# Performance work log

Hardware: AMD Instinct MI355X
Metric: run time of the kernel (lower is better)

## Reference

```python
import jax, jax.numpy as jnp
import numpy as np

HEADS = 8
DIM_HEAD = 64
CHUNK = 128
EPS = 1e-6
KERNEL_EPS = 1e-4


def softmax_kernel(x, proj, is_query):
    # x: [b,h,n,d], proj: [f,d]  (FAVOR+ positive softmax features)
    d = x.shape[-1]
    data_normalizer = d ** -0.25
    ratio = proj.shape[0] ** -0.5
    data_dash = jnp.einsum('bhnd,fd->bhnf', x * data_normalizer, proj)
    diag = 0.5 * (data_normalizer ** 2) * jnp.sum(x * x, axis=-1, keepdims=True)  # [b,h,n,1]
    if is_query:
        m = jnp.max(data_dash, axis=-1, keepdims=True)
    else:
        m = jnp.max(data_dash, axis=(-1, -2), keepdims=True)
    return ratio * (jnp.exp(data_dash - diag - jax.lax.stop_gradient(m)) + KERNEL_EPS)


def infer_hidden_states(q, k, v, chunk_size=CHUNK):
    # q,k: [b,h,n,f], v: [b,h,n,e]; chunked causal linear attention with carried cumsums
    b, h, n, f = q.shape
    e = v.shape[-1]
    nc = n // chunk_size

    def to_chunks(t):
        return jnp.moveaxis(t.reshape(b, h, nc, chunk_size, t.shape[-1]), 2, 0)

    qs, ks, vs = to_chunks(q), to_chunks(k), to_chunks(v)

    def step(carry, inp):
        Z, S = carry  # [b,h,1,f], [b,h,1,f,e]
        qc, kc, vc = inp
        k_cum = Z + jnp.cumsum(kc, axis=2)                       # [b,h,c,f]
        D_inv = 1.0 / jnp.einsum('bhnf,bhnf->bhn', qc, k_cum + EPS)
        ctx = jnp.einsum('bhnf,bhne->bhnfe', kc, vc)             # [b,h,c,f,e]
        ctx_cum = S + jnp.cumsum(ctx, axis=2)
        out = jnp.einsum('bhnfe,bhnf,bhn->bhne', ctx_cum, qc, D_inv)
        return (k_cum[:, :, -1:], ctx_cum[:, :, -1:]), out

    init = (jnp.zeros((b, h, 1, f), q.dtype), jnp.zeros((b, h, 1, f, e), q.dtype))
    (Z, S), outs = jax.lax.scan(step, init, (qs, ks, vs))
    out = jnp.moveaxis(outs, 0, 2).reshape(b, h, n, e)
    return out, Z[:, :, 0], S[:, :, 0]


def reference(x, proj, Wq, Wk, Wv, Wo, bo):
    b, n, dim = x.shape
    h, dh = HEADS, DIM_HEAD

    def split_heads(t):
        return jnp.transpose(t.reshape(b, n, h, dh), (0, 2, 1, 3))

    q = split_heads(x @ Wq)
    k = split_heads(x @ Wk)
    v = split_heads(x @ Wv)

    qf = softmax_kernel(q, proj, is_query=True)
    kf = softmax_kernel(k, proj, is_query=False)

    out, Z, S = infer_hidden_states(qf, kf, v)
    out = jnp.transpose(out, (0, 2, 1, 3)).reshape(b, n, h * dh)
    out = out @ Wo + bo
    return out, Z, S


def setup_inputs() -> dict:
    key = jax.random.key(0)
    ks = jax.random.split(key, 6)
    b, n, dim = 2, 2048, 512
    f = 256
    return {
        'x': jax.random.normal(ks[0], (b, n, dim), jnp.float32),
        'proj': jax.random.normal(ks[1], (f, DIM_HEAD), jnp.float32),
        'Wq': jax.random.normal(ks[2], (dim, dim), jnp.float32) * (dim ** -0.5),
        'Wk': jax.random.normal(ks[3], (dim, dim), jnp.float32) * (dim ** -0.5),
        'Wv': jax.random.normal(ks[4], (dim, dim), jnp.float32) * (dim ** -0.5),
        'Wo': jax.random.normal(ks[5], (dim, dim), jnp.float32) * (dim ** -0.5),
        'bo': jnp.zeros((dim,), jnp.float32),
    }
```

## Files before the change

kernel.cpp:

```cpp
#include <hip/hip_runtime.h>
#include <hip/hip_bf16.h>
#include <math.h>

#define NB    2
#define NSEQ  2048
#define DIMM  512
#define NH    8
#define DHd   64
#define FF    256
#define CHK   128
#define NCHK  16
#define NBH   16

typedef unsigned short ushort_t;
typedef __attribute__((ext_vector_type(8))) __bf16 bf16x8;
typedef __attribute__((ext_vector_type(4))) float floatx4;

__device__ __forceinline__ unsigned short f2bf(float x) {
    union { __hip_bfloat16 h; unsigned short u; } v;
    v.h = __float2bfloat16(x);
    return v.u;
}
__device__ __forceinline__ float bf2f(unsigned short u) {
    union { unsigned short u2[2]; float f; } v;
    v.u2[0] = 0; v.u2[1] = u;
    return v.f;
}
__device__ __forceinline__ unsigned enc_f(float x) {
    unsigned u = __float_as_uint(x);
    return (u & 0x80000000u) ? ~u : (u | 0x80000000u);
}
__device__ __forceinline__ float dec_f(unsigned e) {
    unsigned u = (e & 0x80000000u) ? (e & 0x7fffffffu) : ~e;
    return __uint_as_float(u);
}

__device__ __forceinline__ void gload16(const void* g, void* l) {
    __builtin_amdgcn_global_load_lds(
        (const __attribute__((address_space(1))) void*)g,
        (__attribute__((address_space(3))) void*)l, 16, 0, 0);
}

__device__ __forceinline__ bf16x8 frag8(const ushort_t* lds, int row, int kb) {
    return *((const bf16x8*)lds + row * 8 + (kb ^ (row & 7)));
}
__device__ __forceinline__ bf16x8 fragS(const ushort_t* lds, int row, int kb) {
    return *((const bf16x8*)lds + row * 16 + (kb ^ (row & 15)));
}

__global__ __launch_bounds__(256)
void prep(const float* __restrict__ x, const float* __restrict__ proj,
          const float* __restrict__ W0, const float* __restrict__ W1,
          const float* __restrict__ W2, const float* __restrict__ W3,
          ushort_t* __restrict__ xb, ushort_t* __restrict__ projb,
          ushort_t* __restrict__ T0, ushort_t* __restrict__ T1,
          ushort_t* __restrict__ T2, ushort_t* __restrict__ T3,
          unsigned* __restrict__ mk_u)
{
    __shared__ float t[32][33];
    const int b = blockIdx.x, tid = threadIdx.x;
    if (b < 2048) {
        const int gid = b * 256 + tid;
        const float4 v = *(const float4*)(x + (size_t)gid * 4);
        union { ushort4 v4; unsigned short s[4]; } pk;
        pk.s[0] = f2bf(v.x); pk.s[1] = f2bf(v.y); pk.s[2] = f2bf(v.z); pk.s[3] = f2bf(v.w);
        ((ushort4*)xb)[gid] = pk.v4;
    } else if (b < 2064) {
        const int gid = (b - 2048) * 256 + tid;
        const float dn = 0.35355339059327379f;
        const float4 v = *(const float4*)(proj + (size_t)gid * 4);
        union { ushort4 v4; unsigned short s[4]; } pk;
        pk.s[0] = f2bf(v.x * dn); pk.s[1] = f2bf(v.y * dn);
        pk.s[2] = f2bf(v.z * dn); pk.s[3] = f2bf(v.w * dn);
        ((ushort4*)projb)[gid] = pk.v4;
    } else if (b < 3088) {
        const int idx = b - 2064;
        const int z = idx >> 8, rem = idx & 255;
        const int bx = rem & 15, by = rem >> 4;
        const float* W = (z == 0) ? W0 : (z == 1) ? W1 : (z == 2) ? W2 : W3;
        ushort_t* T = (z == 0) ? T0 : (z == 1) ? T1 : (z == 2) ? T2 : T3;
        const int x0 = bx * 32, y0 = by * 32;
        const int tx = tid & 31, ty = tid >> 5;
#pragma unroll
        for (int i = 0; i < 4; i++)
            t[ty + i * 8][tx] = W[(size_t)(y0 + ty + i * 8) * DIMM + x0 + tx];
        __syncthreads();
#pragma unroll
        for (int i = 0; i < 4; i++)
            T[(size_t)(x0 + ty + i * 8) * DIMM + y0 + tx] = f2bf(t[tx][ty + i * 8]);
    } else {
        if (tid < NBH) mk_u[tid] = 0u;
    }
}

__device__ __forceinline__ void mfma_mainloop(
    const ushort_t* __restrict__ AG, const ushort_t* __restrict__ BG,
    ushort_t* As, ushort_t* Bs, int ldA, int ldB, int K,
    floatx4 acc[4][4], int tid)
{
    const int lane = tid & 63, wid = tid >> 6;
    const int q = lane >> 4, c = lane & 15;
    const int wm = (wid >> 1) * 64, wn = (wid & 1) * 64;

    for (int k0 = 0; k0 < K; k0 += 64) {
#pragma unroll
        for (int t = 0; t < 4; t++) {
            const int g = t * 256 + tid, r = g >> 3, kb = (g & 7) ^ (r & 7);
            gload16(AG + (size_t)r * ldA + k0 + kb * 8, As + (size_t)g * 8);
        }
#pragma unroll
        for (int t = 0; t < 4; t++) {
            const int g = t * 256 + tid, r = g >> 3, kb = (g & 7) ^ (r & 7);
            gload16(BG + (size_t)r * ldB + k0 + kb * 8, Bs + (size_t)g * 8);
        }
        __syncthreads();
#pragma unroll
        for (int ks = 0; ks < 2; ks++) {
            bf16x8 af[4], bfr[4];
#pragma unroll
            for (int i = 0; i < 4; i++) {
                af[i]  = frag8(As, wm + i * 16 + c, ks * 4 + q);
                bfr[i] = frag8(Bs, wn + i * 16 + c, ks * 4 + q);
            }
#pragma unroll
            for (int i = 0; i < 4; i++)
#pragma unroll
                for (int j = 0; j < 4; j++)
                    acc[i][j] = __builtin_amdgcn_mfma_f32_16x16x32_bf16(
                        af[i], bfr[j], acc[i][j], 0, 0, 0);
        }
        __syncthreads();
    }
}

__global__ __launch_bounds__(256)
void gemm_qkv(const ushort_t* __restrict__ xb,
              const ushort_t* __restrict__ Wtq, const ushort_t* __restrict__ Wtk,
              const ushort_t* __restrict__ Wtv,
              ushort_t* __restrict__ qb, ushort_t* __restrict__ kb,
              ushort_t* __restrict__ vTb)
{
    __shared__ alignas(16) ushort_t SM[16896];
    ushort_t* As = SM;
    ushort_t* Bs = SM + 8192;
    const int tid = threadIdx.x;
    const int n0 = blockIdx.x * 128, m0 = blockIdx.y * 128, z = blockIdx.z;
    const ushort_t* Bt = (z == 0) ? Wtq : ((z == 1) ? Wtk : Wtv);

    floatx4 zero = {0.f, 0.f, 0.f, 0.f};
    floatx4 acc[4][4];
#pragma unroll
    for (int i = 0; i < 4; i++)
#pragma unroll
        for (int j = 0; j < 4; j++) acc[i][j] = zero;

    mfma_mainloop(xb + (size_t)m0 * DIMM, Bt + (size_t)n0 * DIMM, As, Bs,
                  DIMM, DIMM, DIMM, acc, tid);

    const int lane = tid & 63, wid = tid >> 6;
    const int q = lane >> 4, c = lane & 15;
    const int wm = (wid >> 1) * 64, wn = (wid & 1) * 64;

#pragma unroll
    for (int i = 0; i < 4; i++)
#pragma unroll
        for (int j = 0; j < 4; j++) {
            const int col = wn + j * 16 + c;
#pragma unroll
            for (int r = 0; r < 4; r++) {
                const int row = wm + i * 16 + q * 4 + r;
                SM[row * 132 + col] = f2bf(acc[i][j][r]);
            }
        }
    __syncthreads();

    if (z < 2) {
        ushort_t* ob = (z == 0) ? qb : kb;
#pragma unroll
        for (int p = 0; p < 16; p++) {
            const int idx = p * 256 + tid;
            const int row = idx >> 5, c4 = idx & 31;
            ushort4 o = *(const ushort4*)&SM[row * 132 + c4 * 4];
            *(ushort4*)(ob + (size_t)(m0 + row) * DIMM + n0 + c4 * 4) = o;
        }
    } else {
        const int bb = m0 >> 11, nbase = m0 & 2047;
#pragma unroll
        for (int p = 0; p < 16; p++) {
            const int idx = p * 256 + tid;
            const int cl2 = idx >> 5, n4 = idx & 31;
            const int C = n0 + cl2;
            const int h = C >> 6, e = C & 63;
            union { ushort4 v4; unsigned short s[4]; } pk;
#pragma unroll
            for (int k = 0; k < 4; k++) pk.s[k] = SM[(n4 * 4 + k) * 132 + cl2];
            *(ushort4*)(vTb + (((size_t)(bb * NH + h) * 64 + e)) * NSEQ + nbase + n4 * 4) = pk.v4;
        }
    }
}

__global__ __launch_bounds__(256)
void gemm_out(const ushort_t* __restrict__ attnb, const ushort_t* __restrict__ Wto,
              float* __restrict__ out, const float* __restrict__ bias)
{
    __shared__ alignas(16) ushort_t As[8192];
    __shared__ alignas(16) ushort_t Bs[8192];
    const int tid = threadIdx.x;
    const int n0 = blockIdx.x * 128, m0 = blockIdx.y * 128;

    floatx4 zero = {0.f, 0.f, 0.f, 0.f};
    floatx4 acc[4][4];
#pragma unroll
    for (int i = 0; i < 4; i++)
#pragma unroll
        for (int j = 0; j < 4; j++) acc[i][j] = zero;

    mfma_mainloop(attnb + (size_t)m0 * DIMM, Wto + (size_t)n0 * DIMM, As, Bs,
                  DIMM, DIMM, DIMM, acc, tid);

    const int lane = tid & 63, wid = tid >> 6;
    const int q = lane >> 4, c = lane & 15;
    const int wm = (wid >> 1) * 64, wn = (wid & 1) * 64;
#pragma unroll
    for (int i = 0; i < 4; i++)
#pragma unroll
        for (int j = 0; j < 4; j++) {
            const int col = n0 + wn + j * 16 + c;
            const float bv = bias[col];
#pragma unroll
            for (int r = 0; r < 4; r++) {
                const int row = m0 + wm + i * 16 + q * 4 + r;
                out[(size_t)row * DIMM + col] = acc[i][j][r] + bv;
            }
        }
}

__global__ __launch_bounds__(256)
void kmax(const ushort_t* __restrict__ kb_, const ushort_t* __restrict__ projb,
          unsigned* __restrict__ mk_u)
{
    __shared__ alignas(16) ushort_t As[8192];
    __shared__ alignas(16) ushort_t Bs[16384];
    __shared__ float red[256];
    const int tid = threadIdx.x, lane = tid & 63, wid = tid >> 6;
    const int q = lane >> 4, cl = lane & 15;
    const int m0 = blockIdx.x * 128, h = blockIdx.y;
    const int bb = m0 >> 11;
    const ushort_t* Aq = kb_ + (size_t)m0 * DIMM + h * 64;

#pragma unroll
    for (int t = 0; t < 4; t++) {
        const int g = t * 256 + tid, r = g >> 3, kb = (g & 7) ^ (r & 7);
        gload16(Aq + (size_t)r * DIMM + kb * 8, As + (size_t)g * 8);
    }
#pragma unroll
    for (int t = 0; t < 8; t++) {
        const int g = t * 256 + tid, r = g >> 3, kb = (g & 7) ^ (r & 7);
        gload16(projb + (size_t)r * 64 + kb * 8, Bs + (size_t)g * 8);
    }
    __syncthreads();

    floatx4 zero = {0.f, 0.f, 0.f, 0.f};
    floatx4 acc[4][8];
#pragma unroll
    for (int i = 0; i < 4; i++)
#pragma unroll
        for (int j = 0; j < 8; j++) acc[i][j] = zero;
    const int wm = (wid >> 1) * 64, wn = (wid & 1) * 128;
#pragma unroll
    for (int ks = 0; ks < 2; ks++) {
        bf16x8 af[4], bfr[8];
#pragma unroll
        for (int i = 0; i < 4; i++) af[i] = frag8(As, wm + i * 16 + cl, ks * 4 + q);
#pragma unroll
        for (int j = 0; j < 8; j++) bfr[j] = frag8(Bs, wn + j * 16 + cl, ks * 4 + q);
#pragma unroll
        for (int i = 0; i < 4; i++)
#pragma unroll
            for (int j = 0; j < 8; j++)
                acc[i][j] = __builtin_amdgcn_mfma_f32_16x16x32_bf16(
                    af[i], bfr[j], acc[i][j], 0, 0, 0);
    }
    float mloc = -3.0e38f;
#pragma unroll
    for (int i = 0; i < 4; i++)
#pragma unroll
        for (int j = 0; j < 8; j++)
#pragma unroll
            for (int r = 0; r < 4; r++) mloc = fmaxf(mloc, acc[i][j][r]);
    red[tid] = mloc;
    __syncthreads();
    for (int s = 128; s > 0; s >>= 1) {
        if (tid < s) red[tid] = fmaxf(red[tid], red[tid + s]);
        __syncthreads();
    }
    if (tid == 0) atomicMax(&mk_u[bb * NH + h], enc_f(red[0]));
}

__global__ __launch_bounds__(256)
void featx(const ushort_t* __restrict__ qb_, const ushort_t* __restrict__ kb_,
           const ushort_t* __restrict__ projb, const unsigned* __restrict__ mk_u,
           const ushort_t* __restrict__ vTb,
           ushort_t* __restrict__ qfb, ushort_t* __restrict__ kfb,
           float* __restrict__ CTXT, float* __restrict__ Ksum)
{
    __shared__ alignas(16) ushort_t SM[24576];
    __shared__ float dtmp[256];
    __shared__ float diag_l[128];
    __shared__ float mx2[2][128];
    __shared__ float colp[2][256];
    ushort_t* As = SM;
    ushort_t* Bs = SM + 8192;
    const int tid = threadIdx.x, lane = tid & 63, wid = tid >> 6;
    const int q = lane >> 4, cl = lane & 15;
    const int m0 = blockIdx.x * 128, h = blockIdx.y, src = blockIdx.z;
    const int bb = m0 >> 11, nloc = m0 & 2047;
    const int bh = bb * NH + h;
    const int cidx = nloc >> 7;
    const ushort_t* Aq = (src ? kb_ : qb_) + (size_t)m0 * DIMM + h * 64;

    {
        const int row = tid >> 1, half = tid & 1;
        float s = 0.f;
        const ushort_t* p = Aq + (size_t)row * DIMM + half * 32;
#pragma unroll
        for (int d = 0; d < 32; d += 4) {
            ushort4 w = *(const ushort4*)(p + d);
            float a = bf2f(w.x), b2 = bf2f(w.y), c2 = bf2f(w.z), d2 = bf2f(w.w);
            s += a * a + b2 * b2 + c2 * c2 + d2 * d2;
        }
        dtmp[tid] = s;
    }
    __syncthreads();
    if (tid < 128) diag_l[tid] = (dtmp[2 * tid] + dtmp[2 * tid + 1]) * 0.0625f;

#pragma unroll
    for (int t = 0; t < 4; t++) {
        const int g = t * 256 + tid, r = g >> 3, kb = (g & 7) ^ (r & 7);
        gload16(Aq + (size_t)r * DIMM + kb * 8, As + (size_t)g * 8);
    }
#pragma unroll
    for (int t = 0; t < 8; t++) {
        const int g = t * 256 + tid, r = g >> 3, kb = (g & 7) ^ (r & 7);
        gload16(projb + (size_t)r * 64 + kb * 8, Bs + (size_t)g * 8);
    }
    __syncthreads();

    floatx4 zero = {0.f, 0.f, 0.f, 0.f};
    floatx4 acc[4][8];
#pragma unroll
    for (int i = 0; i < 4; i++)
#pragma unroll
        for (int j = 0; j < 8; j++) acc[i][j] = zero;
    const int wm = (wid >> 1) * 64, wn = (wid & 1) * 128;
#pragma unroll
    for (int ks = 0; ks < 2; ks++) {
        bf16x8 af[4], bfr[8];
#pragma unroll
        for (int i = 0; i < 4; i++) af[i] = frag8(As, wm + i * 16 + cl, ks * 4 + q);
#pragma unroll
        for (int j = 0; j < 8; j++) bfr[j] = frag8(Bs, wn + j * 16 + cl, ks * 4 + q);
#pragma unroll
        for (int i = 0; i < 4; i++)
#pragma unroll
            for (int j = 0; j < 8; j++)
                acc[i][j] = __builtin_amdgcn_mfma_f32_16x16x32_bf16(
                    af[i], bfr[j], acc[i][j], 0, 0, 0);
    }

    const float mk = src ? dec_f(mk_u[bh]) : 0.f;
    if (src == 0) {
#pragma unroll
        for (int i = 0; i < 4; i++)
#pragma unroll
            for (int r = 0; r < 4; r++) {
                const int row = wm + i * 16 + q * 4 + r;
                float mx = -3.0e38f;
#pragma unroll
                for (int j = 0; j < 8; j++) mx = fmaxf(mx, acc[i][j][r]);
                mx = fmaxf(mx, __shfl_xor(mx, 1)); mx = fmaxf(mx, __shfl_xor(mx, 2));
                mx = fmaxf(mx, __shfl_xor(mx, 4)); mx = fmaxf(mx, __shfl_xor(mx, 8));
                if (cl == 0) mx2[wid & 1][row] = mx;
            }
    }
    __syncthreads();

#pragma unroll
    for (int i = 0; i < 4; i++)
#pragma unroll
        for (int r = 0; r < 4; r++) {
            const int row = wm + i * 16 + q * 4 + r;
            const float cc = diag_l[row] + (src ? mk : fmaxf(mx2[0][row], mx2[1][row]));
#pragma unroll
            for (int j = 0; j < 8; j++)
                acc[i][j][r] = 0.0625f * (__expf(acc[i][j][r] - cc) + 1.0e-4f);
        }

    if (src) {
#pragma unroll
        for (int j = 0; j < 8; j++) {
            float s = 0.f;
#pragma unroll
            for (int i = 0; i < 4; i++)
                s += acc[i][j][0] + acc[i][j][1] + acc[i][j][2] + acc[i][j][3];
            s += __shfl_xor(s, 16);
            s += __shfl_xor(s, 32);
            if (q == 0) colp[wid >> 1][wn + j * 16 + cl] = s;
        }
    }

    ushort_t* ff = src ? kfb : qfb;
    const size_t frow = (size_t)bh * NSEQ + nloc;

#pragma unroll
    for (int hf = 0; hf < 2; hf++) {
        __syncthreads();
        if ((wid & 1) == hf) {
#pragma unroll
            for (int i = 0; i < 4; i++)
#pragma unroll
                for (int j = 0; j < 8; j++) {
                    const int col = j * 16 + cl;
#pragma unroll
                    for (int r = 0; r < 4; r++) {
                        const int row = wm + i * 16 + q * 4 + r;
                        SM[row * 132 + col] = f2bf(acc[i][j][r]);
                    }
                }
        }
        if (hf == 0 && src) {
            Ksum[((size_t)bh * NCHK + cidx) * FF + tid] = colp[0][tid] + colp[1][tid];
        }
        __syncthreads();
#pragma unroll
        for (int p = 0; p < 16; p++) {
            const int idx = p * 256 + tid;
            const int row = idx >> 5, c4 = idx & 31;
            ushort4 o = *(const ushort4*)&SM[row * 132 + c4 * 4];
            *(ushort4*)(ff + (frow + row) * FF + hf * 128 + c4 * 4) = o;
        }
    }

    if (src == 0) return;

    __syncthreads();
    ushort_t* Vs = SM;
    ushort_t* T  = SM + 8192;
    const ushort_t* Vg = vTb + ((size_t)bh * 64) * NSEQ + nloc;
#pragma unroll
    for (int t = 0; t < 4; t++) {
        const int g = t * 256 + tid, r = g >> 4, kb = (g & 15) ^ (r & 15);
        gload16(Vg + (size_t)r * NSEQ + kb * 8, Vs + (size_t)g * 8);
    }

    const size_t cbase = ((size_t)bh * NCHK + cidx) * 64;
#pragma unroll
    for (int fq = 0; fq < 4; fq++) {
        if ((wid & 1) == (fq >> 1)) {
#pragma unroll
            for (int jj = 0; jj < 4; jj++) {
                const int j = (fq & 1) * 4 + jj;
#pragma unroll
                for (int i = 0; i < 4; i++)
#pragma unroll
                    for (int r = 0; r < 4; r++) {
                        const int n = wm + i * 16 + q * 4 + r;
                        T[(jj * 16 + cl) * 136 + n] = f2bf(acc[i][j][r]);
                    }
            }
        }
        __syncthreads();
        floatx4 accc[4];
#pragma unroll
        for (int jj = 0; jj < 4; jj++) accc[jj] = zero;
#pragma unroll
        for (int kt = 0; kt < 4; kt++) {
            const bf16x8 av = fragS(Vs, wid * 16 + cl, kt * 4 + q);
#pragma unroll
            for (int jj = 0; jj < 4; jj++) {
                const bf16x8 bv = *(const bf16x8*)(T + (jj * 16 + cl) * 136 + (kt * 4 + q) * 8);
                accc[jj] = __builtin_amdgcn_mfma_f32_16x16x32_bf16(av, bv, accc[jj], 0, 0, 0);
            }
        }
#pragma unroll
        for (int jj = 0; jj < 4; jj++) {
            const int f = fq * 64 + jj * 16 + cl;
#pragma unroll
            for (int r = 0; r < 4; r++) {
                const int e = wid * 16 + q * 4 + r;
                CTXT[(cbase + e) * FF + f] = accc[jj][r];
            }
        }
        __syncthreads();
    }
}

__global__ void prefix_zs(float* __restrict__ Ksum, float* __restrict__ Zout,
                          const float* __restrict__ CTXT, ushort_t* __restrict__ ctxp,
                          float* __restrict__ Sout)
{
    const int b = blockIdx.x;
    if (b < 1024) {
        const int idx = b * 256 + threadIdx.x;
        const int bh = idx >> 14, ef = idx & 16383;
        const int e = ef >> 8, f = ef & 255;
        float run = 0.f;
#pragma unroll
        for (int c = 0; c < NCHK; c++) {
            const size_t o = (((size_t)bh * NCHK + c) * 64 + e) * FF + f;
            const float t = CTXT[o];
            ctxp[o] = f2bf(run);
            run += t;
        }
        Sout[((size_t)bh * FF + f) * 64 + e] = run;
    } else {
        const int idx = (b - 1024) * 256 + threadIdx.x;
        const int bh = idx >> 8, f = idx & 255;
        float run = 0.f;
#pragma unroll
        for (int c = 0; c < NCHK; c++) {
            const size_t o = ((size_t)(bh * NCHK + c)) * FF + f;
            const float t = Ksum[o];
            Ksum[o] = run;
            run += t;
        }
        Zout[(size_t)bh * FF + f] = run;
    }
}

__global__ __launch_bounds__(256)
void chunk_out_mfma(const ushort_t* __restrict__ qfb, const ushort_t* __restrict__ kfb,
                    const ushort_t* __restrict__ vTb, const float* __restrict__ Zex,
                    const ushort_t* __restrict__ ctxp, ushort_t* __restrict__ attnb)
{
    __shared__ alignas(16) ushort_t Sld[16384];
    __shared__ alignas(16) ushort_t As[8192];
    __shared__ alignas(16) ushort_t Bs[8192];
    __shared__ float zeps[256];
    __shared__ float rows_part[2][128];
    __shared__ float denp[256];
    __shared__ float den_l[128];

    const int tid = threadIdx.x, lane = tid & 63, wid = tid >> 6;
    const int q = lane >> 4, cl = lane & 15;
    const int bh = blockIdx.x >> 4, c = blockIdx.x & 15;
    const int bb = bh >> 3, h = bh & 7;
    const int n0 = c * CHK;
    const ushort_t* Q  = qfb + ((size_t)bh * NSEQ + n0) * FF;
    const ushort_t* Kf = kfb + ((size_t)bh * NSEQ + n0) * FF;

    zeps[tid] = Zex[((size_t)bh * NCHK + c) * FF + tid] + 1.0e-6f;

    floatx4 zero = {0.f, 0.f, 0.f, 0.f};
    floatx4 acc1[4][4];
#pragma unroll
    for (int i = 0; i < 4; i++)
#pragma unroll
        for (int j = 0; j < 4; j++) acc1[i][j] = zero;
    const int wm = (wid >> 1) * 64, wn = (wid & 1) * 64;
    for (int k0 = 0; k0 < FF; k0 += 64) {
#pragma unroll
        for (int t = 0; t < 4; t++) {
            const int g = t * 256 + tid, r = g >> 3, kb = (g & 7) ^ (r & 7);
            gload16(Q + (size_t)r * FF + k0 + kb * 8, As + (size_t)g * 8);
        }
#pragma unroll
        for (int t = 0; t < 4; t++) {
            const int g = t * 256 + tid, r = g >> 3, kb = (g & 7) ^ (r & 7);
            gload16(Kf + (size_t)r * FF + k0 + kb * 8, Bs + (size_t)g * 8);
        }
        __syncthreads();
#pragma unroll
        for (int ks = 0; ks < 2; ks++) {
            bf16x8 af[4], bfr[4];
#pragma unroll
            for (int i = 0; i < 4; i++) {
                af[i]  = frag8(As, wm + i * 16 + cl, ks * 4 + q);
                bfr[i] = frag8(Bs, wn + i * 16 + cl, ks * 4 + q);
            }
#pragma unroll
            for (int i = 0; i < 4; i++)
#pragma unroll
                for (int j = 0; j < 4; j++)
                    acc1[i][j] = __builtin_amdgcn_mfma_f32_16x16x32_bf16(
                        af[i], bfr[j], acc1[i][j], 0, 0, 0);
        }
        __syncthreads();
    }
#pragma unroll
    for (int i = 0; i < 4; i++)
#pragma unroll
        for (int r = 0; r < 4; r++) {
            const int row = wm + i * 16 + q * 4 + r;
            float part = 0.f;
#pragma unroll
            for (int j = 0; j < 4; j++) {
                const int col = wn + j * 16 + cl;
                const float v = (col <= row) ? acc1[i][j][r] : 0.f;
                part += v;
                Sld[(row * 16 + ((col >> 3) ^ (row & 15))) * 8 + (col & 7)] = f2bf(v);
            }
            part += __shfl_xor(part, 1); part += __shfl_xor(part, 2);
            part += __shfl_xor(part, 4); part += __shfl_xor(part, 8);
            if (cl == 0) rows_part[wid & 1][row] = part;
        }
    __syncthreads();

    floatx4 acc2[4][2];
#pragma unroll
    for (int i = 0; i < 4; i++)
#pragma unroll
        for (int j = 0; j < 2; j++) acc2[i][j] = zero;
    const ushort_t* Vt = vTb + ((size_t)bh * 64) * NSEQ + n0;
    for (int k0 = 0; k0 < CHK; k0 += 64) {
#pragma unroll
        for (int t = 0; t < 2; t++) {
            const int g = t * 256 + tid, r = g >> 3, kb = (g & 7) ^ (r & 7);
            gload16(Vt + (size_t)r * NSEQ + k0 + kb * 8, As + (size_t)g * 8);
        }
        __syncthreads();
#pragma unroll
        for (int ks = 0; ks < 2; ks++) {
            bf16x8 af[4], bfr[2];
            const int kbS = (k0 >> 3) + ks * 4 + q;
#pragma unroll
            for (int i = 0; i < 4; i++) af[i] = frag8(As, i * 16 + cl, ks * 4 + q);
#pragma unroll
            for (int j = 0; j < 2; j++) bfr[j] = fragS(Sld, wid * 32 + j * 16 + cl, kbS);
#pragma unroll
            for (int i = 0; i < 4; i++)
#pragma unroll
                for (int j = 0; j < 2; j++)
                    acc2[i][j] = __builtin_amdgcn_mfma_f32_16x16x32_bf16(
                        af[i], bfr[j], acc2[i][j], 0, 0, 0);
        }
        __syncthreads();
    }

    const ushort_t* Cp = ctxp + ((size_t)bh * NCHK + c) * 64 * FF;
    float dacc = 0.f;
    const int drow = tid & 127, dhalf = tid >> 7;
    for (int k0 = 0; k0 < FF; k0 += 64) {
#pragma unroll
        for (int t = 0; t < 2; t++) {
            const int g = t * 256 + tid, r = g >> 3, kb = (g & 7) ^ (r & 7);
            gload16(Cp + (size_t)r * FF + k0 + kb * 8, As + (size_t)g * 8);
        }
#pragma unroll
        for (int t = 0; t < 4; t++) {
            const int g = t * 256 + tid, r = g >> 3, kb = (g & 7) ^ (r & 7);
            gload16(Q + (size_t)r * FF + k0 + kb * 8, Bs + (size_t)g * 8);
        }
        __syncthreads();
#pragma unroll
        for (int ks = 0; ks < 2; ks++) {
            bf16x8 af[4], bfr[2];
#pragma unroll
            for (int i = 0; i < 4; i++) af[i] = frag8(As, i * 16 + cl, ks * 4 + q);
#pragma unroll
            for (int j = 0; j < 2; j++) bfr[j] = frag8(Bs, wid * 32 + j * 16 + cl, ks * 4 + q);
#pragma unroll
            for (int i = 0; i < 4; i++)
#pragma unroll
                for (int j = 0; j < 2; j++)
                    acc2[i][j] = __builtin_amdgcn_mfma_f32_16x16x32_bf16(
                        af[i], bfr[j], acc2[i][j], 0, 0, 0);
        }
#pragma unroll
        for (int gi = 0; gi < 4; gi++) {
            const int kb = dhalf * 4 + gi;
            const ushort_t* gp = Bs + ((size_t)drow * 8 + (kb ^ (drow & 7))) * 8;
            const int kbase = k0 + kb * 8;
#pragma unroll
            for (int e2 = 0; e2 < 8; e2++)
                dacc = fmaf(bf2f(gp[e2]), zeps[kbase + e2], dacc);
        }
        __syncthreads();
    }
    denp[tid] = dacc;
    __syncthreads();
    if (tid < 128)
        den_l[tid] = rows_part[0][tid] + rows_part[1][tid] + denp[tid] + denp[tid + 128];
    __syncthreads();

#pragma unroll
    for (int j = 0; j < 2; j++) {
        const int row = wid * 32 + j * 16 + cl;
        const float dinv = 1.0f / den_l[row];
#pragma unroll
        for (int i = 0; i < 4; i++)
#pragma unroll
            for (int r = 0; r < 4; r++) {
                const int e = i * 16 + q * 4 + r;
                Sld[row * 68 + e] = f2bf(acc2[i][j][r] * dinv);
            }
    }
    __syncthreads();
#pragma unroll
    for (int p = 0; p < 8; p++) {
        const int idx = p * 256 + tid;
        const int row = idx >> 4, e4 = idx & 15;
        ushort4 o = *(const ushort4*)&Sld[row * 68 + e4 * 4];
        *(ushort4*)(attnb + ((size_t)(bb * NSEQ + n0 + row)) * DIMM + h * 64 + e4 * 4) = o;
    }
}

extern "C" void kernel_launch(void* const* d_in, const int* in_sizes, int n_in,
                              void* d_out, int out_size, void* d_ws, size_t ws_size,
                              hipStream_t stream)
{
    (void)in_sizes; (void)n_in; (void)out_size; (void)ws_size;
    const float* x    = (const float*)d_in[0];
    const float* proj = (const float*)d_in[1];
    const float* Wq   = (const float*)d_in[2];
    const float* Wk   = (const float*)d_in[3];
    const float* Wv   = (const float*)d_in[4];
    const float* Wo   = (const float*)d_in[5];
    const float* bo   = (const float*)d_in[6];
    float* out = (float*)d_out;

    char* W = (char*)d_ws;
    float*    CTXT = (float*)W;              W += (size_t)16777216;
    ushort_t* qfb  = (ushort_t*)W;           W += (size_t)16777216;
    ushort_t* kfb  = (ushort_t*)W;           W += (size_t)16777216;
    ushort_t* qb   = (ushort_t*)W;           W += (size_t)4194304;
    ushort_t* kb   = (ushort_t*)W;           W += (size_t)4194304;
    ushort_t* xb   = (ushort_t*)W;           W += (size_t)4194304;
    ushort_t* vTb  = (ushort_t*)W;           W += (size_t)4194304;
    ushort_t* Wtq  = (ushort_t*)W;           W += (size_t)524288;
    ushort_t* Wtk  = (ushort_t*)W;           W += (size_t)524288;
    ushort_t* Wtv  = (ushort_t*)W;           W += (size_t)524288;
    ushort_t* Wto  = (ushort_t*)W;           W += (size_t)524288;
    ushort_t* projb = (ushort_t*)W;          W += (size_t)32768;
    float*    Ksum = (float*)W;              W += (size_t)262144;
    unsigned* mk_u = (unsigned*)W;           W += (size_t)256;

    ushort_t* ctxp = qb;
    ushort_t* attnb = xb;

    float* Zout = out + (size_t)4096 * 512;
    float* Sout = Zout + (size_t)NBH * FF;

    hipLaunchKernelGGL(prep, dim3(3089), dim3(256), 0, stream,
                       x, proj, Wq, Wk, Wv, Wo, xb, projb, Wtq, Wtk, Wtv, Wto, mk_u);
    hipLaunchKernelGGL(gemm_qkv, dim3(4, 32, 3), dim3(256), 0, stream,
                       xb, Wtq, Wtk, Wtv, qb, kb, vTb);
    hipLaunchKernelGGL(kmax, dim3(32, 8), dim3(256), 0, stream, kb, projb, mk_u);
    hipLaunchKernelGGL(featx, dim3(32, 8, 2), dim3(256), 0, stream,
                       qb, kb, projb, mk_u, vTb, qfb, kfb, CTXT, Ksum);
    hipLaunchKernelGGL(prefix_zs, dim3(1040), dim3(256), 0, stream,
                       Ksum, Zout, CTXT, ctxp, Sout);
    hipLaunchKernelGGL(chunk_out_mfma, dim3(256), dim3(256), 0, stream,
                       qfb, kfb, vTb, Ksum, ctxp, attnb);
    hipLaunchKernelGGL(gemm_out, dim3(4, 32), dim3(256), 0, stream, attnb, Wto, out, bo);
}
```

Baseline: 157.3 us.

## Fuse key max-reduction projection into QKV GEMM epilogue, drop kmax kernel

The separate kmax kernel, which reloaded k from global memory and multiplied it by the projection to find the per-head global max, is removed. Its work now runs in the epilogue of the z==1 (key) blocks of gemm_qkv, reusing the bf16 k tile already held in shared memory and loading proj in two halves. This saves one launch and one global read of k. In exchange the key blocks carry a longer epilogue with extra syncs, and the shared-memory footprint grows, which may lower occupancy and leave the q and v blocks waiting on the slower k blocks.

```diff
diff --git a/kernel.cpp b/kernel.cpp
--- a/kernel.cpp
+++ b/kernel.cpp
@@ -136,13 +136,15 @@
 __global__ __launch_bounds__(256)
 void gemm_qkv(const ushort_t* __restrict__ xb,
               const ushort_t* __restrict__ Wtq, const ushort_t* __restrict__ Wtk,
-              const ushort_t* __restrict__ Wtv,
+              const ushort_t* __restrict__ Wtv, const ushort_t* __restrict__ projb,
               ushort_t* __restrict__ qb, ushort_t* __restrict__ kb,
-              ushort_t* __restrict__ vTb)
+              ushort_t* __restrict__ vTb, unsigned* __restrict__ mk_u)
 {
-    __shared__ alignas(16) ushort_t SM[16896];
+    __shared__ alignas(16) ushort_t SM[25600];
+    __shared__ float red[256];
     ushort_t* As = SM;
     ushort_t* Bs = SM + 8192;
+    ushort_t* PS = SM + 17408;
     const int tid = threadIdx.x;
     const int n0 = blockIdx.x * 128, m0 = blockIdx.y * 128, z = blockIdx.z;
     const ushort_t* Bt = (z == 0) ? Wtq : ((z == 1) ? Wtk : Wtv);
@@ -158,30 +160,95 @@
                   DIMM, DIMM, DIMM, acc, tid);
 
     const int lane = tid & 63, wid = tid >> 6;
-    const int q = lane >> 4, c = lane & 15;
+    const int q = lane >> 4, cl = lane & 15;
     const int wm = (wid >> 1) * 64, wn = (wid & 1) * 64;
 
 #pragma unroll
     for (int i = 0; i < 4; i++)
 #pragma unroll
         for (int j = 0; j < 4; j++) {
-            const int col = wn + j * 16 + c;
+            const int col = wn + j * 16 + cl;
 #pragma unroll
             for (int r = 0; r < 4; r++) {
                 const int row = wm + i * 16 + q * 4 + r;
-                SM[row * 132 + col] = f2bf(acc[i][j][r]);
+                SM[row * 136 + col] = f2bf(acc[i][j][r]);
             }
         }
     __syncthreads();
 
     if (z < 2) {
         ushort_t* ob = (z == 0) ? qb : kb;
+        if (z == 1) {
+#pragma unroll
+            for (int t = 0; t < 4; t++) {
+                const int g = t * 256 + tid, f = g >> 3, kbg = (g & 7) ^ (f & 7);
+                gload16(projb + (size_t)f * 64 + kbg * 8, PS + (size_t)g * 8);
+            }
+        }
 #pragma unroll
         for (int p = 0; p < 16; p++) {
             const int idx = p * 256 + tid;
             const int row = idx >> 5, c4 = idx & 31;
-            ushort4 o = *(const ushort4*)&SM[row * 132 + c4 * 4];
+            ushort4 o = *(const ushort4*)&SM[row * 136 + c4 * 4];
             *(ushort4*)(ob + (size_t)(m0 + row) * DIMM + n0 + c4 * 4) = o;
+        }
+        if (z == 1) {
+            const int bb = m0 >> 11;
+            const int h0 = n0 >> 6;
+            float mx[2] = {-3.0e38f, -3.0e38f};
+#pragma unroll
+            for (int half = 0; half < 2; half++) {
+                __syncthreads();
+#pragma unroll
+                for (int hh = 0; hh < 2; hh++) {
+                    floatx4 a2[4][4];
+#pragma unroll
+                    for (int i = 0; i < 4; i++)
+#pragma unroll
+                        for (int j = 0; j < 4; j++) a2[i][j] = zero;
+#pragma unroll
+                    for (int ks = 0; ks < 2; ks++) {
+                        bf16x8 af[4], bfr[4];
+#pragma unroll
+                        for (int i = 0; i < 4; i++)
+                            af[i] = *(const bf16x8*)&SM[(wm + i * 16 + cl) * 136 + hh * 64 + (ks * 4 + q) * 8];
+#pragma unroll
+                        for (int j = 0; j < 4; j++)
+                            bfr[j] = frag8(PS, wn + j * 16 + cl, ks * 4 + q);
+#pragma unroll
+                        for (int i = 0; i < 4; i++)
+#pragma unroll
+                            for (int j = 0; j < 4; j++)
+                                a2[i][j] = __builtin_amdgcn_mfma_f32_16x16x32_bf16(
+                                    af[i], bfr[j], a2[i][j], 0, 0, 0);
+                    }
+#pragma unroll
+                    for (int i = 0; i < 4; i++)
+#pragma unroll
+                        for (int j = 0; j < 4; j++)
+#pragma unroll
+                            for (int r = 0; r < 4; r++) mx[hh] = fmaxf(mx[hh], a2[i][j][r]);
+                }
+                if (half == 0) {
+                    __syncthreads();
+#pragma unroll
+                    for (int t = 0; t < 4; t++) {
+                        const int g = t * 256 + tid, f = g >> 3, kbg = (g & 7) ^ (f & 7);
+                        gload16(projb + (size_t)(128 + f) * 64 + kbg * 8, PS + (size_t)g * 8);
+                    }
+                }
+            }
+#pragma unroll
+            for (int hh = 0; hh < 2; hh++) {
+                __syncthreads();
+                red[tid] = mx[hh];
+                __syncthreads();
+                for (int s = 128; s > 0; s >>= 1) {
+                    if (tid < s) red[tid] = fmaxf(red[tid], red[tid + s]);
+                    __syncthreads();
+                }
+                if (tid == 0) atomicMax(&mk_u[bb * NH + h0 + hh], enc_f(red[0]));
+            }
         }
     } else {
         const int bb = m0 >> 11, nbase = m0 & 2047;
@@ -193,7 +260,7 @@
             const int h = C >> 6, e = C & 63;
             union { ushort4 v4; unsigned short s[4]; } pk;
 #pragma unroll
-            for (int k = 0; k < 4; k++) pk.s[k] = SM[(n4 * 4 + k) * 132 + cl2];
+            for (int k = 0; k < 4; k++) pk.s[k] = SM[(n4 * 4 + k) * 136 + cl2];
             *(ushort4*)(vTb + (((size_t)(bb * NH + h) * 64 + e)) * NSEQ + nbase + n4 * 4) = pk.v4;
         }
     }
@@ -233,68 +300,6 @@
                 out[(size_t)row * DIMM + col] = acc[i][j][r] + bv;
             }
         }
-}
-
-__global__ __launch_bounds__(256)
-void kmax(const ushort_t* __restrict__ kb_, const ushort_t* __restrict__ projb,
-          unsigned* __restrict__ mk_u)
-{
-    __shared__ alignas(16) ushort_t As[8192];
-    __shared__ alignas(16) ushort_t Bs[16384];
-    __shared__ float red[256];
-    const int tid = threadIdx.x, lane = tid & 63, wid = tid >> 6;
-    const int q = lane >> 4, cl = lane & 15;
-    const int m0 = blockIdx.x * 128, h = blockIdx.y;
-    const int bb = m0 >> 11;
-    const ushort_t* Aq = kb_ + (size_t)m0 * DIMM + h * 64;
-
-#pragma unroll
-    for (int t = 0; t < 4; t++) {
-        const int g = t * 256 + tid, r = g >> 3, kb = (g & 7) ^ (r & 7);
-        gload16(Aq + (size_t)r * DIMM + kb * 8, As + (size_t)g * 8);
-    }
-#pragma unroll
-    for (int t = 0; t < 8; t++) {
-        const int g = t * 256 + tid, r = g >> 3, kb = (g & 7) ^ (r & 7);
-        gload16(projb + (size_t)r * 64 + kb * 8, Bs + (size_t)g * 8);
-    }
-    __syncthreads();
-
-    floatx4 zero = {0.f, 0.f, 0.f, 0.f};
-    floatx4 acc[4][8];
-#pragma unroll
-    for (int i = 0; i < 4; i++)
-#pragma unroll
-        for (int j = 0; j < 8; j++) acc[i][j] = zero;
-    const int wm = (wid >> 1) * 64, wn = (wid & 1) * 128;
-#pragma unroll
-    for (int ks = 0; ks < 2; ks++) {
-        bf16x8 af[4], bfr[8];
-#pragma unroll
-        for (int i = 0; i < 4; i++) af[i] = frag8(As, wm + i * 16 + cl, ks * 4 + q);
-#pragma unroll
-        for (int j = 0; j < 8; j++) bfr[j] = frag8(Bs, wn + j * 16 + cl, ks * 4 + q);
-#pragma unroll
-        for (int i = 0; i < 4; i++)
-#pragma unroll
-            for (int j = 0; j < 8; j++)
-                acc[i][j] = __builtin_amdgcn_mfma_f32_16x16x32_bf16(
-                    af[i], bfr[j], acc[i][j], 0, 0, 0);
-    }
-    float mloc = -3.0e38f;
-#pragma unroll
-    for (int i = 0; i < 4; i++)
-#pragma unroll
-        for (int j = 0; j < 8; j++)
-#pragma unroll
-            for (int r = 0; r < 4; r++) mloc = fmaxf(mloc, acc[i][j][r]);
-    red[tid] = mloc;
-    __syncthreads();
-    for (int s = 128; s > 0; s >>= 1) {
-        if (tid < s) red[tid] = fmaxf(red[tid], red[tid + s]);
-        __syncthreads();
-    }
-    if (tid == 0) atomicMax(&mk_u[bb * NH + h], enc_f(red[0]));
 }
 
 __global__ __launch_bounds__(256)
@@ -744,8 +749,7 @@
     hipLaunchKernelGGL(prep, dim3(3089), dim3(256), 0, stream,
                        x, proj, Wq, Wk, Wv, Wo, xb, projb, Wtq, Wtk, Wtv, Wto, mk_u);
     hipLaunchKernelGGL(gemm_qkv, dim3(4, 32, 3), dim3(256), 0, stream,
-                       xb, Wtq, Wtk, Wtv, qb, kb, vTb);
-    hipLaunchKernelGGL(kmax, dim3(32, 8), dim3(256), 0, stream, kb, projb, mk_u);
+                       xb, Wtq, Wtk, Wtv, projb, qb, kb, vTb, mk_u);
     hipLaunchKernelGGL(featx, dim3(32, 8, 2), dim3(256), 0, stream,
                        qb, kb, projb, mk_u, vTb, qfb, kfb, CTXT, Ksum);
     hipLaunchKernelGGL(prefix_zs, dim3(1040), dim3(256), 0, stream,
```

New measurement: 155.6 us. No clear change (-1.1%).
